# Optimization experiments

Measured on AMD Instinct MI355X. Metric: run time of the kernel, lower is better.

Reference implementation:

```python
import jax, jax.numpy as jnp
import numpy as np

S, B, E, H = 2048, 2, 1024, 16
HD = E // H


def setup_inputs() -> dict:
    key = jax.random.key(0)
    ks = jax.random.split(key, 8)
    sc = 0.05
    return {
        "query": jax.random.normal(ks[0], (S, B, E), jnp.float32),
        "key": jax.random.normal(ks[1], (S, B, E), jnp.float32),
        "value": jax.random.normal(ks[2], (S, B, E), jnp.float32),
        "position_bias": jax.random.normal(ks[3], (B, S, S), jnp.float32) * sc,
        "in_proj_weight": jax.random.normal(ks[4], (3 * E, E), jnp.float32) * sc,
        "in_proj_bias": jnp.zeros((3 * E,), jnp.float32),
        "out_w": jax.random.normal(ks[5], (E, E), jnp.float32) * sc,
        "out_b": jnp.zeros((E,), jnp.float32),
    }


def reference(query, key, value, position_bias, in_proj_weight, in_proj_bias, out_w, out_b):
    # packed in-projection: w is (3E, E) in q,k,v order
    w_q, w_k, w_v = jnp.split(in_proj_weight, 3, axis=0)
    b_q, b_k, b_v = jnp.split(in_proj_bias, 3, axis=0)
    q = query @ w_q.T + b_q          # (S, B, E)
    k = key @ w_k.T + b_k
    v = value @ w_v.T + b_v
    # split heads: (S, B, H, HD)
    q = q.reshape(S, B, H, HD)
    k = k.reshape(S, B, H, HD)
    v = v.reshape(S, B, H, HD)
    scale = 1.0 / jnp.sqrt(jnp.float32(HD))
    # scores: (B, H, tgt, src)
    scores = jnp.einsum("qbhd,kbhd->bhqk", q * scale, k)
    scores = scores + position_bias[:, None, :, :]
    attn = jax.nn.softmax(scores, axis=-1)
    out = jnp.einsum("bhqk,kbhd->qbhd", attn, v).reshape(S, B, E)
    out = out @ out_w.T + out_b      # (S, B, E)
    attn_weights = attn.reshape(B * H, S, S)
    return out, attn_weights
```

## Files before the change

kernel.cpp:

```cpp
#include <hip/hip_runtime.h>

#define S_ 2048
#define B_ 2
#define E_ 1024
#define H_ 16

typedef _Float16 f16x8 __attribute__((ext_vector_type(8)));
typedef _Float16 f16x4 __attribute__((ext_vector_type(4)));
typedef _Float16 f16x2 __attribute__((ext_vector_type(2)));
typedef float f32x4 __attribute__((ext_vector_type(4)));
typedef unsigned short us4_t __attribute__((ext_vector_type(4)));
typedef unsigned u32x4 __attribute__((ext_vector_type(4)));
typedef unsigned u32x2 __attribute__((ext_vector_type(2)));

static __device__ __forceinline__ unsigned short f2h(float x) {
  _Float16 h = (_Float16)x;
  return __builtin_bit_cast(unsigned short, h);
}
static __device__ __forceinline__ unsigned pk_f16(float a, float b) {
  auto r = __builtin_amdgcn_cvt_pkrtz(a, b);
  return __builtin_bit_cast(unsigned, r);
}

__global__ void k_cvth(const float* __restrict__ src, unsigned short* __restrict__ dst, int n4) {
  int i = blockIdx.x * blockDim.x + threadIdx.x;
  int st = gridDim.x * blockDim.x;
  for (; i < n4; i += st) {
    f32x4 x = ((const f32x4*)src)[i];
    us4_t h;
    #pragma unroll
    for (int j = 0; j < 4; ++j) h[j] = f2h(x[j]);
    ((us4_t*)dst)[i] = h;
  }
}

__launch_bounds__(256, 2)
__global__ void k_proj_qk(const unsigned short* __restrict__ qx, const unsigned short* __restrict__ kx,
                          const unsigned short* __restrict__ wqk, const float* __restrict__ bias,
                          unsigned short* __restrict__ qf, unsigned short* __restrict__ kf) {
  const int z = blockIdx.z;
  const unsigned short* A = z ? kx : qx;
  const unsigned short* W = wqk + (size_t)z * (1024 * 1024);
  unsigned short* C = z ? kf : qf;
  const float* bia = bias + z * 1024;
  const float scale = z ? 1.0f : 0.125f;

  __shared__ unsigned short sA[128][40], sB[128][40];

  const int t = threadIdx.x;
  const int wid = t >> 6, l = t & 63, g = l >> 4, c = l & 15;
  const int wr = wid >> 1, wc = wid & 1;
  const int mb = blockIdx.x * 128, nb = blockIdx.y * 128;
  const int sr = t >> 1, sc = (t & 1) * 16;

  f32x4 acc[4][4] = {};

  for (int k0 = 0; k0 < 1024; k0 += 32) {
    __syncthreads();
    {
      const unsigned short* pa = A + (size_t)(mb + sr) * 1024 + k0 + sc;
      const unsigned short* pb = W + (size_t)(nb + sr) * 1024 + k0 + sc;
      *(f16x8*)&sA[sr][sc]     = *(const f16x8*)pa;
      *(f16x8*)&sA[sr][sc + 8] = *(const f16x8*)(pa + 8);
      *(f16x8*)&sB[sr][sc]     = *(const f16x8*)pb;
      *(f16x8*)&sB[sr][sc + 8] = *(const f16x8*)(pb + 8);
    }
    __syncthreads();
    f16x8 af[4], bf[4];
    #pragma unroll
    for (int i = 0; i < 4; ++i) {
      af[i] = *(const f16x8*)&sA[wr * 64 + i * 16 + c][g * 8];
      bf[i] = *(const f16x8*)&sB[wc * 64 + i * 16 + c][g * 8];
    }
    #pragma unroll
    for (int i = 0; i < 4; ++i)
      #pragma unroll
      for (int j = 0; j < 4; ++j)
        acc[i][j] = __builtin_amdgcn_mfma_f32_16x16x32_f16(af[i], bf[j], acc[i][j], 0, 0, 0);
  }
  #pragma unroll
  for (int i = 0; i < 4; ++i)
    #pragma unroll
    for (int j = 0; j < 4; ++j)
      #pragma unroll
      for (int rr = 0; rr < 4; ++rr) {
        int m = mb + wr * 64 + i * 16 + 4 * g + rr;
        int n = nb + wc * 64 + j * 16 + c;
        float v = (acc[i][j][rr] + bia[n]) * scale;
        C[(size_t)m * 1024 + n] = f2h(v);
      }
}

__launch_bounds__(256, 2)
__global__ void k_proj_v(const unsigned short* __restrict__ wv, const unsigned short* __restrict__ vx,
                         const float* __restrict__ bias, unsigned short* __restrict__ VT) {
  __shared__ unsigned short sA[128][40], sB[128][40];
  const int t = threadIdx.x;
  const int wid = t >> 6, l = t & 63, g = l >> 4, c = l & 15;
  const int wr = wid >> 1, wc = wid & 1;
  const int mb = blockIdx.x * 128;
  const int nb = blockIdx.y * 128;
  const int bb = nb >> 11;
  const int jb = nb & 2047;
  const int sr = t >> 1, sc = (t & 1) * 16;

  f32x4 acc[4][4] = {};
  for (int k0 = 0; k0 < 1024; k0 += 32) {
    __syncthreads();
    {
      const unsigned short* pa = wv + (size_t)(mb + sr) * 1024 + k0 + sc;
      const unsigned short* pb = vx + ((size_t)(jb + sr) * 2 + bb) * 1024 + k0 + sc;
      *(f16x8*)&sA[sr][sc]     = *(const f16x8*)pa;
      *(f16x8*)&sA[sr][sc + 8] = *(const f16x8*)(pa + 8);
      *(f16x8*)&sB[sr][sc]     = *(const f16x8*)pb;
      *(f16x8*)&sB[sr][sc + 8] = *(const f16x8*)(pb + 8);
    }
    __syncthreads();
    f16x8 af[4], bf[4];
    #pragma unroll
    for (int i = 0; i < 4; ++i) {
      af[i] = *(const f16x8*)&sA[wr * 64 + i * 16 + c][g * 8];
      bf[i] = *(const f16x8*)&sB[wc * 64 + i * 16 + c][g * 8];
    }
    #pragma unroll
    for (int i = 0; i < 4; ++i)
      #pragma unroll
      for (int j = 0; j < 4; ++j)
        acc[i][j] = __builtin_amdgcn_mfma_f32_16x16x32_f16(af[i], bf[j], acc[i][j], 0, 0, 0);
  }
  #pragma unroll
  for (int i = 0; i < 4; ++i)
    #pragma unroll
    for (int j = 0; j < 4; ++j)
      #pragma unroll
      for (int rr = 0; rr < 4; ++rr) {
        int m = mb + wr * 64 + i * 16 + 4 * g + rr;
        int jj = jb + wc * 64 + j * 16 + c;
        float v = acc[i][j][rr] + bias[2048 + m];
        VT[(size_t)bb * (1024 * 2048) + (size_t)m * 2048 + jj] = f2h(v);
      }
}

__launch_bounds__(256, 3)
__global__ void k_attn_pv(const unsigned short* __restrict__ qf, const unsigned short* __restrict__ kf,
                          const unsigned short* __restrict__ VT, const float* __restrict__ posb,
                          float* __restrict__ attn, unsigned short* __restrict__ oc) {
  const int swz = (int)((blockIdx.x & 7) * 512 + (blockIdx.x >> 3));
  const int h = swz >> 8;
  const int b = (swz >> 7) & 1;
  const int qt = swz & 127;

  const int t = threadIdx.x;
  const int wid = t >> 6, l = t & 63, g = l >> 4, c = l & 15;
  const int ct = wid;

  __shared__ unsigned smem[8192];
  __shared__ float lds_red[4][16];
  unsigned* S_k = smem;
  unsigned* S_v = smem + 4096;

  const size_t qoff = ((size_t)(qt * 16 + c) * 2 + b) * 1024 + h * 64 + g * 8;
  const f16x8 qfr0 = *(const f16x8*)(qf + qoff);
  const f16x8 qfr1 = *(const f16x8*)(qf + qoff + 32);

  const unsigned short* kfb = kf + (size_t)b * 1024 + h * 64;
  const unsigned short* vtb = VT + ((size_t)b * 1024 + h * 64) * 2048;
  const float* pbRow = posb + (size_t)b * S_ * S_ + (size_t)(qt * 16 + c) * S_ + ct * 16;

  const int rb = t >> 3;
  const int lsl = (t & 7) ^ (rb & 7);

  #define LDSRD(base, row, slot) \
    __builtin_bit_cast(f16x8, *(const u32x4*)&(base)[(row) * 32 + ((((slot) ^ ((row) & 7))) * 4)])

  #define GLOAD(dst, stg) do { \
    dst[0] = *(const u32x4*)(kfb + (size_t)((stg) * 64 + rb) * 2048 + lsl * 8); \
    dst[1] = *(const u32x4*)(kfb + (size_t)((stg) * 64 + rb + 32) * 2048 + lsl * 8); \
    dst[2] = *(const u32x4*)(vtb + (size_t)rb * 2048 + (stg) * 64 + lsl * 8); \
    dst[3] = *(const u32x4*)(vtb + (size_t)(rb + 32) * 2048 + (stg) * 64 + lsl * 8); \
  } while (0)

  #define SWRITE(src, buf) do { \
    *(u32x4*)&S_k[(buf) * 2048 + t * 4]        = src[0]; \
    *(u32x4*)&S_k[(buf) * 2048 + 1024 + t * 4] = src[1]; \
    *(u32x4*)&S_v[(buf) * 2048 + t * 4]        = src[2]; \
    *(u32x4*)&S_v[(buf) * 2048 + 1024 + t * 4] = src[3]; \
  } while (0)

  u32x4 rg[3][4];
  f32x4 bias[2];
  unsigned psc0[32], psc1[32];
  float lsum = 0.f;
  f32x4 oacc[4] = {};

  GLOAD(rg[0], 0);
  SWRITE(rg[0], 0);
  GLOAD(rg[1], 1);
  GLOAD(rg[2], 2);
  {
    f32x4 b0 = *(const f32x4*)(pbRow + 4 * g);
    bias[0][0] = b0[0] - 8.f; bias[0][1] = b0[1] - 8.f;
    bias[0][2] = b0[2] - 8.f; bias[0][3] = b0[3] - 8.f;
  }
  __syncthreads();

  #pragma unroll
  for (int st = 0; st < 32; ++st) {
    const int cur = st & 1;
    if (st < 29) GLOAD(rg[st % 3], st + 3);
    if (st < 31) {
      f32x4 bb = *(const f32x4*)(pbRow + (st + 1) * 64 + 4 * g);
      bias[cur ^ 1][0] = bb[0] - 8.f; bias[cur ^ 1][1] = bb[1] - 8.f;
      bias[cur ^ 1][2] = bb[2] - 8.f; bias[cur ^ 1][3] = bb[3] - 8.f;
    }

    {
      const int row = ct * 16 + c;
      const unsigned* kb = S_k + cur * 2048;
      f16x8 kfr0 = LDSRD(kb, row, g);
      f16x8 kfr1 = LDSRD(kb, row, 4 + g);
      f32x4 aA = {}, aB = {};
      aA = __builtin_amdgcn_mfma_f32_16x16x32_f16(kfr0, qfr0, aA, 0, 0, 0);
      aB = __builtin_amdgcn_mfma_f32_16x16x32_f16(kfr1, qfr1, aB, 0, 0, 0);
      float p0 = __expf(aA[0] + aB[0] + bias[cur][0]);
      float p1 = __expf(aA[1] + aB[1] + bias[cur][1]);
      float p2 = __expf(aA[2] + aB[2] + bias[cur][2]);
      float p3 = __expf(aA[3] + aB[3] + bias[cur][3]);
      lsum += (p0 + p1) + (p2 + p3);
      psc0[st] = pk_f16(p0, p1);
      psc1[st] = pk_f16(p2, p3);
    }

    {
      u32x2 br; br[0] = psc0[st]; br[1] = psc1[st];
      const f16x4 bfrag = __builtin_bit_cast(f16x4, br);
      const unsigned* vb = S_v + cur * 2048;
      #pragma unroll
      for (int dt = 0; dt < 4; ++dt) {
        const int row = dt * 16 + c;
        const int sl = (2 * ct + (g >> 1)) ^ (row & 7);
        u32x2 ar = *(const u32x2*)&vb[row * 32 + sl * 4 + 2 * (g & 1)];
        f32x4 o = oacc[dt];
#if __has_builtin(__builtin_amdgcn_mfma_f32_16x16x16f16)
        o = __builtin_amdgcn_mfma_f32_16x16x16f16(__builtin_bit_cast(f16x4, ar), bfrag, o, 0, 0, 0);
#else
        asm("v_mfma_f32_16x16x16_f16 %0, %1, %2, %0" : "+v"(o) : "v"(__builtin_bit_cast(f16x4, ar)), "v"(bfrag));
#endif
        oacc[dt] = o;
      }
    }

    if (st < 31) SWRITE(rg[(st + 1) % 3], cur ^ 1);
    __syncthreads();
  }

  lsum += __shfl_xor(lsum, 16, 64);
  lsum += __shfl_xor(lsum, 32, 64);
  if (l < 16) lds_red[wid][l] = lsum;
  __syncthreads();
  const float inv = 1.0f / ((lds_red[0][c] + lds_red[1][c]) + (lds_red[2][c] + lds_red[3][c]));

  float* ored = (float*)smem;
  #pragma unroll
  for (int dt = 0; dt < 4; ++dt) {
    f32x4 o = oacc[dt];
    o[0] *= inv; o[1] *= inv; o[2] *= inv; o[3] *= inv;
    *(f32x4*)&ored[(wid * 16 + c) * 68 + dt * 16 + 4 * g] = o;
  }
  __syncthreads();
  {
    const int q = t >> 4;
    const int d0 = (t & 15) * 4;
    f32x4 s0 = *(const f32x4*)&ored[(0 * 16 + q) * 68 + d0];
    f32x4 s1 = *(const f32x4*)&ored[(1 * 16 + q) * 68 + d0];
    f32x4 s2 = *(const f32x4*)&ored[(2 * 16 + q) * 68 + d0];
    f32x4 s3 = *(const f32x4*)&ored[(3 * 16 + q) * 68 + d0];
    f32x4 s;
    s[0] = (s0[0] + s1[0]) + (s2[0] + s3[0]);
    s[1] = (s0[1] + s1[1]) + (s2[1] + s3[1]);
    s[2] = (s0[2] + s1[2]) + (s2[2] + s3[2]);
    s[3] = (s0[3] + s1[3]) + (s2[3] + s3[3]);
    u32x2 pk;
    pk[0] = pk_f16(s[0], s[1]);
    pk[1] = pk_f16(s[2], s[3]);
    *(u32x2*)&oc[((size_t)(qt * 16 + q) * 2 + b) * 1024 + h * 64 + d0] = pk;
  }

  float* arow = attn + ((size_t)(b * 16 + h) * S_ + qt * 16 + c) * S_ + ct * 16;
  #pragma unroll
  for (int st = 0; st < 32; ++st) {
    f16x2 h0 = __builtin_bit_cast(f16x2, psc0[st]);
    f16x2 h1 = __builtin_bit_cast(f16x2, psc1[st]);
    f32x4 o;
    o[0] = (float)h0[0] * inv;
    o[1] = (float)h0[1] * inv;
    o[2] = (float)h1[0] * inv;
    o[3] = (float)h1[1] * inv;
    *(f32x4*)(arow + (size_t)st * 64 + 4 * g) = o;
  }
  #undef LDSRD
  #undef GLOAD
  #undef SWRITE
}

__launch_bounds__(256, 2)
__global__ void k_outproj(const unsigned short* __restrict__ oc, const unsigned short* __restrict__ ow,
                          const float* __restrict__ ob, float* __restrict__ out) {
  __shared__ unsigned short sA[128][40], sB[128][40];
  const int t = threadIdx.x;
  const int wid = t >> 6, l = t & 63, g = l >> 4, c = l & 15;
  const int wr = wid >> 1, wc = wid & 1;
  const int mb = blockIdx.x * 128, nb = blockIdx.y * 128;
  const int sr = t >> 1, sc = (t & 1) * 16;

  f32x4 acc[4][4] = {};
  for (int k0 = 0; k0 < 1024; k0 += 32) {
    __syncthreads();
    {
      const unsigned short* pa = oc + (size_t)(mb + sr) * 1024 + k0 + sc;
      const unsigned short* pb = ow + (size_t)(nb + sr) * 1024 + k0 + sc;
      *(f16x8*)&sA[sr][sc]     = *(const f16x8*)pa;
      *(f16x8*)&sA[sr][sc + 8] = *(const f16x8*)(pa + 8);
      *(f16x8*)&sB[sr][sc]     = *(const f16x8*)pb;
      *(f16x8*)&sB[sr][sc + 8] = *(const f16x8*)(pb + 8);
    }
    __syncthreads();
    f16x8 af[4], bf[4];
    #pragma unroll
    for (int i = 0; i < 4; ++i) {
      af[i] = *(const f16x8*)&sA[wr * 64 + i * 16 + c][g * 8];
      bf[i] = *(const f16x8*)&sB[wc * 64 + i * 16 + c][g * 8];
    }
    #pragma unroll
    for (int i = 0; i < 4; ++i)
      #pragma unroll
      for (int j = 0; j < 4; ++j)
        acc[i][j] = __builtin_amdgcn_mfma_f32_16x16x32_f16(af[i], bf[j], acc[i][j], 0, 0, 0);
  }
  #pragma unroll
  for (int i = 0; i < 4; ++i)
    #pragma unroll
    for (int j = 0; j < 4; ++j)
      #pragma unroll
      for (int rr = 0; rr < 4; ++rr) {
        int m = mb + wr * 64 + i * 16 + 4 * g + rr;
        int n = nb + wc * 64 + j * 16 + c;
        out[(size_t)m * 1024 + n] = acc[i][j][rr] + ob[n];
      }
}

extern "C" void kernel_launch(void* const* d_in, const int* in_sizes, int n_in,
                              void* d_out, int out_size, void* d_ws, size_t ws_size,
                              hipStream_t stream) {
  (void)in_sizes; (void)n_in; (void)out_size; (void)ws_size;
  const float* query = (const float*)d_in[0];
  const float* keyi  = (const float*)d_in[1];
  const float* value = (const float*)d_in[2];
  const float* posb  = (const float*)d_in[3];
  const float* ipw   = (const float*)d_in[4];
  const float* ipb   = (const float*)d_in[5];
  const float* outw  = (const float*)d_in[6];
  const float* outb  = (const float*)d_in[7];
  float* out = (float*)d_out;
  float* attn = out + (size_t)S_ * B_ * E_;

  char* ws = (char*)d_ws;
  size_t off = 0;
  auto alloc = [&](size_t bytes) -> void* {
    void* p = ws + off;
    off += (bytes + 255) & ~(size_t)255;
    return p;
  };
  const size_t NTOK = (size_t)S_ * B_;
  unsigned short* qx  = (unsigned short*)alloc(NTOK * 1024 * 2);
  unsigned short* kx  = (unsigned short*)alloc(NTOK * 1024 * 2);
  unsigned short* vx  = (unsigned short*)alloc(NTOK * 1024 * 2);
  unsigned short* wqk = (unsigned short*)alloc((size_t)2048 * 1024 * 2);
  unsigned short* wv  = (unsigned short*)alloc((size_t)1024 * 1024 * 2);
  unsigned short* ow  = (unsigned short*)alloc((size_t)1024 * 1024 * 2);
  unsigned short* qf  = (unsigned short*)alloc(NTOK * 1024 * 2);
  unsigned short* kf  = (unsigned short*)alloc(NTOK * 1024 * 2);
  unsigned short* VT  = (unsigned short*)alloc((size_t)2 * 1024 * 2048 * 2);
  unsigned short* oc  = (unsigned short*)alloc(NTOK * 1024 * 2);

  const int n1_4 = (int)(NTOK * 1024 / 4);
  k_cvth<<<2048, 256, 0, stream>>>(query, qx, n1_4);
  k_cvth<<<2048, 256, 0, stream>>>(keyi, kx, n1_4);
  k_cvth<<<2048, 256, 0, stream>>>(value, vx, n1_4);
  k_cvth<<<1024, 256, 0, stream>>>(ipw, wqk, 2048 * 1024 / 4);
  k_cvth<<<512, 256, 0, stream>>>(ipw + 2048 * 1024, wv, 1024 * 1024 / 4);
  k_cvth<<<512, 256, 0, stream>>>(outw, ow, 1024 * 1024 / 4);

  k_proj_qk<<<dim3(32, 8, 2), 256, 0, stream>>>(qx, kx, wqk, ipb, qf, kf);
  k_proj_v<<<dim3(8, 32), 256, 0, stream>>>(wv, vx, ipb, VT);
  k_attn_pv<<<4096, 256, 0, stream>>>(qf, kf, VT, posb, attn, oc);
  k_outproj<<<dim3(32, 8), 256, 0, stream>>>(oc, ow, outb, out);
}
```

Measured before the change: 378.3 us.

## Fuse fp32-to-fp16 conversion into GEMM loads and defer PV step in attention

```diff
diff --git a/kernel.cpp b/kernel.cpp
--- a/kernel.cpp
+++ b/kernel.cpp
@@ -22,25 +22,24 @@
   return __builtin_bit_cast(unsigned, r);
 }
 
-__global__ void k_cvth(const float* __restrict__ src, unsigned short* __restrict__ dst, int n4) {
-  int i = blockIdx.x * blockDim.x + threadIdx.x;
-  int st = gridDim.x * blockDim.x;
-  for (; i < n4; i += st) {
-    f32x4 x = ((const f32x4*)src)[i];
-    us4_t h;
-    #pragma unroll
-    for (int j = 0; j < 4; ++j) h[j] = f2h(x[j]);
-    ((us4_t*)dst)[i] = h;
-  }
+static __device__ __forceinline__ void cvt16(const float* __restrict__ p, unsigned* dst) {
+  f32x4 a0 = *(const f32x4*)p;
+  f32x4 a1 = *(const f32x4*)(p + 4);
+  f32x4 a2 = *(const f32x4*)(p + 8);
+  f32x4 a3 = *(const f32x4*)(p + 12);
+  dst[0] = pk_f16(a0[0], a0[1]); dst[1] = pk_f16(a0[2], a0[3]);
+  dst[2] = pk_f16(a1[0], a1[1]); dst[3] = pk_f16(a1[2], a1[3]);
+  dst[4] = pk_f16(a2[0], a2[1]); dst[5] = pk_f16(a2[2], a2[3]);
+  dst[6] = pk_f16(a3[0], a3[1]); dst[7] = pk_f16(a3[2], a3[3]);
 }
 
 __launch_bounds__(256, 2)
-__global__ void k_proj_qk(const unsigned short* __restrict__ qx, const unsigned short* __restrict__ kx,
-                          const unsigned short* __restrict__ wqk, const float* __restrict__ bias,
+__global__ void k_proj_qk(const float* __restrict__ query, const float* __restrict__ keyi,
+                          const float* __restrict__ ipw, const float* __restrict__ bias,
                           unsigned short* __restrict__ qf, unsigned short* __restrict__ kf) {
   const int z = blockIdx.z;
-  const unsigned short* A = z ? kx : qx;
-  const unsigned short* W = wqk + (size_t)z * (1024 * 1024);
+  const float* A = z ? keyi : query;
+  const float* W = ipw + (size_t)z * (1024 * 1024);
   unsigned short* C = z ? kf : qf;
   const float* bia = bias + z * 1024;
   const float scale = z ? 1.0f : 0.125f;
@@ -58,12 +57,13 @@
   for (int k0 = 0; k0 < 1024; k0 += 32) {
     __syncthreads();
     {
-      const unsigned short* pa = A + (size_t)(mb + sr) * 1024 + k0 + sc;
-      const unsigned short* pb = W + (size_t)(nb + sr) * 1024 + k0 + sc;
-      *(f16x8*)&sA[sr][sc]     = *(const f16x8*)pa;
-      *(f16x8*)&sA[sr][sc + 8] = *(const f16x8*)(pa + 8);
-      *(f16x8*)&sB[sr][sc]     = *(const f16x8*)pb;
-      *(f16x8*)&sB[sr][sc + 8] = *(const f16x8*)(pb + 8);
+      unsigned ap[8], bp[8];
+      cvt16(A + (size_t)(mb + sr) * 1024 + k0 + sc, ap);
+      cvt16(W + (size_t)(nb + sr) * 1024 + k0 + sc, bp);
+      *(u32x4*)&sA[sr][sc]     = *(u32x4*)&ap[0];
+      *(u32x4*)&sA[sr][sc + 8] = *(u32x4*)&ap[4];
+      *(u32x4*)&sB[sr][sc]     = *(u32x4*)&bp[0];
+      *(u32x4*)&sB[sr][sc + 8] = *(u32x4*)&bp[4];
     }
     __syncthreads();
     f16x8 af[4], bf[4];
@@ -92,7 +92,7 @@
 }
 
 __launch_bounds__(256, 2)
-__global__ void k_proj_v(const unsigned short* __restrict__ wv, const unsigned short* __restrict__ vx,
+__global__ void k_proj_v(const float* __restrict__ ipw, const float* __restrict__ value,
                          const float* __restrict__ bias, unsigned short* __restrict__ VT) {
   __shared__ unsigned short sA[128][40], sB[128][40];
   const int t = threadIdx.x;
@@ -103,17 +103,19 @@
   const int bb = nb >> 11;
   const int jb = nb & 2047;
   const int sr = t >> 1, sc = (t & 1) * 16;
+  const float* wv = ipw + (size_t)2048 * 1024;
 
   f32x4 acc[4][4] = {};
   for (int k0 = 0; k0 < 1024; k0 += 32) {
     __syncthreads();
     {
-      const unsigned short* pa = wv + (size_t)(mb + sr) * 1024 + k0 + sc;
-      const unsigned short* pb = vx + ((size_t)(jb + sr) * 2 + bb) * 1024 + k0 + sc;
-      *(f16x8*)&sA[sr][sc]     = *(const f16x8*)pa;
-      *(f16x8*)&sA[sr][sc + 8] = *(const f16x8*)(pa + 8);
-      *(f16x8*)&sB[sr][sc]     = *(const f16x8*)pb;
-      *(f16x8*)&sB[sr][sc + 8] = *(const f16x8*)(pb + 8);
+      unsigned ap[8], bp[8];
+      cvt16(wv + (size_t)(mb + sr) * 1024 + k0 + sc, ap);
+      cvt16(value + ((size_t)(jb + sr) * 2 + bb) * 1024 + k0 + sc, bp);
+      *(u32x4*)&sA[sr][sc]     = *(u32x4*)&ap[0];
+      *(u32x4*)&sA[sr][sc + 8] = *(u32x4*)&ap[4];
+      *(u32x4*)&sB[sr][sc]     = *(u32x4*)&bp[0];
+      *(u32x4*)&sB[sr][sc + 8] = *(u32x4*)&bp[4];
     }
     __syncthreads();
     f16x8 af[4], bf[4];
@@ -154,7 +156,7 @@
   const int wid = t >> 6, l = t & 63, g = l >> 4, c = l & 15;
   const int ct = wid;
 
-  __shared__ unsigned smem[8192];
+  __shared__ unsigned smem[10240];
   __shared__ float lds_red[4][16];
   unsigned* S_k = smem;
   unsigned* S_v = smem + 4096;
@@ -180,11 +182,11 @@
     dst[3] = *(const u32x4*)(vtb + (size_t)(rb + 32) * 2048 + (stg) * 64 + lsl * 8); \
   } while (0)
 
-  #define SWRITE(src, buf) do { \
-    *(u32x4*)&S_k[(buf) * 2048 + t * 4]        = src[0]; \
-    *(u32x4*)&S_k[(buf) * 2048 + 1024 + t * 4] = src[1]; \
-    *(u32x4*)&S_v[(buf) * 2048 + t * 4]        = src[2]; \
-    *(u32x4*)&S_v[(buf) * 2048 + 1024 + t * 4] = src[3]; \
+  #define SWRITE(src, kbuf, vbuf) do { \
+    *(u32x4*)&S_k[(kbuf) * 2048 + t * 4]        = src[0]; \
+    *(u32x4*)&S_k[(kbuf) * 2048 + 1024 + t * 4] = src[1]; \
+    *(u32x4*)&S_v[(vbuf) * 2048 + t * 4]        = src[2]; \
+    *(u32x4*)&S_v[(vbuf) * 2048 + 1024 + t * 4] = src[3]; \
   } while (0)
 
   u32x4 rg[3][4];
@@ -193,8 +195,21 @@
   float lsum = 0.f;
   f32x4 oacc[4] = {};
 
+  #define PVSTEP(i) do { \
+    u32x2 br_; br_[0] = psc0[i]; br_[1] = psc1[i]; \
+    const f16x4 bfrag_ = __builtin_bit_cast(f16x4, br_); \
+    const unsigned* vb_ = S_v + ((i) % 3) * 2048; \
+    _Pragma("unroll") \
+    for (int dt = 0; dt < 4; ++dt) { \
+      const int row_ = dt * 16 + c; \
+      const int sl_ = (2 * ct + (g >> 1)) ^ (row_ & 7); \
+      u32x2 ar_ = *(const u32x2*)&vb_[row_ * 32 + sl_ * 4 + 2 * (g & 1)]; \
+      oacc[dt] = __builtin_amdgcn_mfma_f32_16x16x16f16(__builtin_bit_cast(f16x4, ar_), bfrag_, oacc[dt], 0, 0, 0); \
+    } \
+  } while (0)
+
   GLOAD(rg[0], 0);
-  SWRITE(rg[0], 0);
+  SWRITE(rg[0], 0, 0);
   GLOAD(rg[1], 1);
   GLOAD(rg[2], 2);
   {
@@ -231,28 +246,12 @@
       psc1[st] = pk_f16(p2, p3);
     }
 
-    {
-      u32x2 br; br[0] = psc0[st]; br[1] = psc1[st];
-      const f16x4 bfrag = __builtin_bit_cast(f16x4, br);
-      const unsigned* vb = S_v + cur * 2048;
-      #pragma unroll
-      for (int dt = 0; dt < 4; ++dt) {
-        const int row = dt * 16 + c;
-        const int sl = (2 * ct + (g >> 1)) ^ (row & 7);
-        u32x2 ar = *(const u32x2*)&vb[row * 32 + sl * 4 + 2 * (g & 1)];
-        f32x4 o = oacc[dt];
-#if __has_builtin(__builtin_amdgcn_mfma_f32_16x16x16f16)
-        o = __builtin_amdgcn_mfma_f32_16x16x16f16(__builtin_bit_cast(f16x4, ar), bfrag, o, 0, 0, 0);
-#else
-        asm("v_mfma_f32_16x16x16_f16 %0, %1, %2, %0" : "+v"(o) : "v"(__builtin_bit_cast(f16x4, ar)), "v"(bfrag));
-#endif
-        oacc[dt] = o;
-      }
-    }
-
-    if (st < 31) SWRITE(rg[(st + 1) % 3], cur ^ 1);
-    __syncthreads();
-  }
+    if (st >= 1) PVSTEP(st - 1);
+
+    if (st < 31) SWRITE(rg[(st + 1) % 3], (st + 1) & 1, (st + 1) % 3);
+    __syncthreads();
+  }
+  PVSTEP(31);
 
   lsum += __shfl_xor(lsum, 16, 64);
   lsum += __shfl_xor(lsum, 32, 64);
@@ -301,10 +300,11 @@
   #undef LDSRD
   #undef GLOAD
   #undef SWRITE
+  #undef PVSTEP
 }
 
 __launch_bounds__(256, 2)
-__global__ void k_outproj(const unsigned short* __restrict__ oc, const unsigned short* __restrict__ ow,
+__global__ void k_outproj(const unsigned short* __restrict__ oc, const float* __restrict__ outw,
                           const float* __restrict__ ob, float* __restrict__ out) {
   __shared__ unsigned short sA[128][40], sB[128][40];
   const int t = threadIdx.x;
@@ -318,11 +318,12 @@
     __syncthreads();
     {
       const unsigned short* pa = oc + (size_t)(mb + sr) * 1024 + k0 + sc;
-      const unsigned short* pb = ow + (size_t)(nb + sr) * 1024 + k0 + sc;
+      unsigned bp[8];
+      cvt16(outw + (size_t)(nb + sr) * 1024 + k0 + sc, bp);
       *(f16x8*)&sA[sr][sc]     = *(const f16x8*)pa;
       *(f16x8*)&sA[sr][sc + 8] = *(const f16x8*)(pa + 8);
-      *(f16x8*)&sB[sr][sc]     = *(const f16x8*)pb;
-      *(f16x8*)&sB[sr][sc + 8] = *(const f16x8*)(pb + 8);
+      *(u32x4*)&sB[sr][sc]     = *(u32x4*)&bp[0];
+      *(u32x4*)&sB[sr][sc + 8] = *(u32x4*)&bp[4];
     }
     __syncthreads();
     f16x8 af[4], bf[4];
@@ -372,27 +373,13 @@
     return p;
   };
   const size_t NTOK = (size_t)S_ * B_;
-  unsigned short* qx  = (unsigned short*)alloc(NTOK * 1024 * 2);
-  unsigned short* kx  = (unsigned short*)alloc(NTOK * 1024 * 2);
-  unsigned short* vx  = (unsigned short*)alloc(NTOK * 1024 * 2);
-  unsigned short* wqk = (unsigned short*)alloc((size_t)2048 * 1024 * 2);
-  unsigned short* wv  = (unsigned short*)alloc((size_t)1024 * 1024 * 2);
-  unsigned short* ow  = (unsigned short*)alloc((size_t)1024 * 1024 * 2);
-  unsigned short* qf  = (unsigned short*)alloc(NTOK * 1024 * 2);
-  unsigned short* kf  = (unsigned short*)alloc(NTOK * 1024 * 2);
-  unsigned short* VT  = (unsigned short*)alloc((size_t)2 * 1024 * 2048 * 2);
-  unsigned short* oc  = (unsigned short*)alloc(NTOK * 1024 * 2);
-
-  const int n1_4 = (int)(NTOK * 1024 / 4);
-  k_cvth<<<2048, 256, 0, stream>>>(query, qx, n1_4);
-  k_cvth<<<2048, 256, 0, stream>>>(keyi, kx, n1_4);
-  k_cvth<<<2048, 256, 0, stream>>>(value, vx, n1_4);
-  k_cvth<<<1024, 256, 0, stream>>>(ipw, wqk, 2048 * 1024 / 4);
-  k_cvth<<<512, 256, 0, stream>>>(ipw + 2048 * 1024, wv, 1024 * 1024 / 4);
-  k_cvth<<<512, 256, 0, stream>>>(outw, ow, 1024 * 1024 / 4);
-
-  k_proj_qk<<<dim3(32, 8, 2), 256, 0, stream>>>(qx, kx, wqk, ipb, qf, kf);
-  k_proj_v<<<dim3(8, 32), 256, 0, stream>>>(wv, vx, ipb, VT);
+  unsigned short* qf = (unsigned short*)alloc(NTOK * 1024 * 2);
+  unsigned short* kf = (unsigned short*)alloc(NTOK * 1024 * 2);
+  unsigned short* VT = (unsigned short*)alloc((size_t)2 * 1024 * 2048 * 2);
+  unsigned short* oc = (unsigned short*)alloc(NTOK * 1024 * 2);
+
+  k_proj_qk<<<dim3(32, 8, 2), 256, 0, stream>>>(query, keyi, ipw, ipb, qf, kf);
+  k_proj_v<<<dim3(8, 32), 256, 0, stream>>>(ipw, value, ipb, VT);
   k_attn_pv<<<4096, 256, 0, stream>>>(qf, kf, VT, posb, attn, oc);
-  k_outproj<<<dim3(32, 8), 256, 0, stream>>>(oc, ow, outb, out);
-}
+  k_outproj<<<dim3(32, 8), 256, 0, stream>>>(oc, outw, outb, out);
+}
```

New measurement: 413.2 us. +9.2%, slower.

## Skew PV MFMA one stage behind QK and triple-buffer V tiles in LDS

Applied to the files above, without the earlier changes.

```diff
diff --git a/kernel.cpp b/kernel.cpp
--- a/kernel.cpp
+++ b/kernel.cpp
@@ -154,7 +154,7 @@
   const int wid = t >> 6, l = t & 63, g = l >> 4, c = l & 15;
   const int ct = wid;
 
-  __shared__ unsigned smem[8192];
+  __shared__ unsigned smem[10240];
   __shared__ float lds_red[4][16];
   unsigned* S_k = smem;
   unsigned* S_v = smem + 4096;
@@ -180,11 +180,11 @@
     dst[3] = *(const u32x4*)(vtb + (size_t)(rb + 32) * 2048 + (stg) * 64 + lsl * 8); \
   } while (0)
 
-  #define SWRITE(src, buf) do { \
-    *(u32x4*)&S_k[(buf) * 2048 + t * 4]        = src[0]; \
-    *(u32x4*)&S_k[(buf) * 2048 + 1024 + t * 4] = src[1]; \
-    *(u32x4*)&S_v[(buf) * 2048 + t * 4]        = src[2]; \
-    *(u32x4*)&S_v[(buf) * 2048 + 1024 + t * 4] = src[3]; \
+  #define SWRITE(src, kbuf, vbuf) do { \
+    *(u32x4*)&S_k[(kbuf) * 2048 + t * 4]        = src[0]; \
+    *(u32x4*)&S_k[(kbuf) * 2048 + 1024 + t * 4] = src[1]; \
+    *(u32x4*)&S_v[(vbuf) * 2048 + t * 4]        = src[2]; \
+    *(u32x4*)&S_v[(vbuf) * 2048 + 1024 + t * 4] = src[3]; \
   } while (0)
 
   u32x4 rg[3][4];
@@ -193,8 +193,21 @@
   float lsum = 0.f;
   f32x4 oacc[4] = {};
 
+  #define PVSTEP(i) do { \
+    u32x2 br_; br_[0] = psc0[i]; br_[1] = psc1[i]; \
+    const f16x4 bfrag_ = __builtin_bit_cast(f16x4, br_); \
+    const unsigned* vb_ = S_v + ((i) % 3) * 2048; \
+    _Pragma("unroll") \
+    for (int dt = 0; dt < 4; ++dt) { \
+      const int row_ = dt * 16 + c; \
+      const int sl_ = (2 * ct + (g >> 1)) ^ (row_ & 7); \
+      u32x2 ar_ = *(const u32x2*)&vb_[row_ * 32 + sl_ * 4 + 2 * (g & 1)]; \
+      oacc[dt] = __builtin_amdgcn_mfma_f32_16x16x16f16(__builtin_bit_cast(f16x4, ar_), bfrag_, oacc[dt], 0, 0, 0); \
+    } \
+  } while (0)
+
   GLOAD(rg[0], 0);
-  SWRITE(rg[0], 0);
+  SWRITE(rg[0], 0, 0);
   GLOAD(rg[1], 1);
   GLOAD(rg[2], 2);
   {
@@ -231,28 +244,12 @@
       psc1[st] = pk_f16(p2, p3);
     }
 
-    {
-      u32x2 br; br[0] = psc0[st]; br[1] = psc1[st];
-      const f16x4 bfrag = __builtin_bit_cast(f16x4, br);
-      const unsigned* vb = S_v + cur * 2048;
-      #pragma unroll
-      for (int dt = 0; dt < 4; ++dt) {
-        const int row = dt * 16 + c;
-        const int sl = (2 * ct + (g >> 1)) ^ (row & 7);
-        u32x2 ar = *(const u32x2*)&vb[row * 32 + sl * 4 + 2 * (g & 1)];
-        f32x4 o = oacc[dt];
-#if __has_builtin(__builtin_amdgcn_mfma_f32_16x16x16f16)
-        o = __builtin_amdgcn_mfma_f32_16x16x16f16(__builtin_bit_cast(f16x4, ar), bfrag, o, 0, 0, 0);
-#else
-        asm("v_mfma_f32_16x16x16_f16 %0, %1, %2, %0" : "+v"(o) : "v"(__builtin_bit_cast(f16x4, ar)), "v"(bfrag));
-#endif
-        oacc[dt] = o;
-      }
-    }
-
-    if (st < 31) SWRITE(rg[(st + 1) % 3], cur ^ 1);
-    __syncthreads();
-  }
+    if (st >= 1) PVSTEP(st - 1);
+
+    if (st < 31) SWRITE(rg[(st + 1) % 3], (st + 1) & 1, (st + 1) % 3);
+    __syncthreads();
+  }
+  PVSTEP(31);
 
   lsum += __shfl_xor(lsum, 16, 64);
   lsum += __shfl_xor(lsum, 32, 64);
@@ -301,6 +298,7 @@
   #undef LDSRD
   #undef GLOAD
   #undef SWRITE
+  #undef PVSTEP
 }
 
 __launch_bounds__(256, 2)
```

New measurement: 386.6 us. +2.2%, slower.

## Use direct global-to-LDS loads in attention and merge conversion kernels

Applied to the files above, without the earlier changes.

```diff
diff --git a/kernel.cpp b/kernel.cpp
--- a/kernel.cpp
+++ b/kernel.cpp
@@ -22,15 +22,29 @@
   return __builtin_bit_cast(unsigned, r);
 }
 
-__global__ void k_cvth(const float* __restrict__ src, unsigned short* __restrict__ dst, int n4) {
+__global__ void k_cvt_all(const float* __restrict__ q, const float* __restrict__ k,
+                          const float* __restrict__ v, const float* __restrict__ ipw,
+                          const float* __restrict__ outw,
+                          unsigned short* __restrict__ qx, unsigned short* __restrict__ kx,
+                          unsigned short* __restrict__ vx, unsigned short* __restrict__ w3,
+                          unsigned short* __restrict__ ow) {
+  const int M1 = 1 << 20;
   int i = blockIdx.x * blockDim.x + threadIdx.x;
-  int st = gridDim.x * blockDim.x;
-  for (; i < n4; i += st) {
-    f32x4 x = ((const f32x4*)src)[i];
+  int stp = gridDim.x * blockDim.x;
+  for (; i < 4 * M1; i += stp) {
+    const float* src;
+    unsigned short* dst;
+    int j;
+    if (i < M1)            { src = q;    dst = qx; j = i; }
+    else if (i < 2 * M1)   { src = k;    dst = kx; j = i - M1; }
+    else if (i < 3 * M1)   { src = v;    dst = vx; j = i - 2 * M1; }
+    else if (i < 3 * M1 + 786432) { src = ipw; dst = w3; j = i - 3 * M1; }
+    else                   { src = outw; dst = ow; j = i - 3 * M1 - 786432; }
+    f32x4 x = ((const f32x4*)src)[j];
     us4_t h;
     #pragma unroll
-    for (int j = 0; j < 4; ++j) h[j] = f2h(x[j]);
-    ((us4_t*)dst)[i] = h;
+    for (int e = 0; e < 4; ++e) h[e] = f2h(x[e]);
+    ((us4_t*)dst)[j] = h;
   }
 }
 
@@ -141,7 +155,7 @@
       }
 }
 
-__launch_bounds__(256, 3)
+__launch_bounds__(256, 4)
 __global__ void k_attn_pv(const unsigned short* __restrict__ qf, const unsigned short* __restrict__ kf,
                           const unsigned short* __restrict__ VT, const float* __restrict__ posb,
                           float* __restrict__ attn, unsigned short* __restrict__ oc) {
@@ -173,30 +187,27 @@
   #define LDSRD(base, row, slot) \
     __builtin_bit_cast(f16x8, *(const u32x4*)&(base)[(row) * 32 + ((((slot) ^ ((row) & 7))) * 4)])
 
-  #define GLOAD(dst, stg) do { \
-    dst[0] = *(const u32x4*)(kfb + (size_t)((stg) * 64 + rb) * 2048 + lsl * 8); \
-    dst[1] = *(const u32x4*)(kfb + (size_t)((stg) * 64 + rb + 32) * 2048 + lsl * 8); \
-    dst[2] = *(const u32x4*)(vtb + (size_t)rb * 2048 + (stg) * 64 + lsl * 8); \
-    dst[3] = *(const u32x4*)(vtb + (size_t)(rb + 32) * 2048 + (stg) * 64 + lsl * 8); \
+  #define GLDS(stg, buf) do { \
+    __builtin_amdgcn_global_load_lds( \
+        (const __attribute__((address_space(1))) unsigned*)(kfb + (size_t)((stg) * 64 + rb) * 2048 + lsl * 8), \
+        (__attribute__((address_space(3))) unsigned*)&S_k[(buf) * 2048 + wid * 256], 16, 0, 0); \
+    __builtin_amdgcn_global_load_lds( \
+        (const __attribute__((address_space(1))) unsigned*)(kfb + (size_t)((stg) * 64 + rb + 32) * 2048 + lsl * 8), \
+        (__attribute__((address_space(3))) unsigned*)&S_k[(buf) * 2048 + 1024 + wid * 256], 16, 0, 0); \
+    __builtin_amdgcn_global_load_lds( \
+        (const __attribute__((address_space(1))) unsigned*)(vtb + (size_t)rb * 2048 + (stg) * 64 + lsl * 8), \
+        (__attribute__((address_space(3))) unsigned*)&S_v[(buf) * 2048 + wid * 256], 16, 0, 0); \
+    __builtin_amdgcn_global_load_lds( \
+        (const __attribute__((address_space(1))) unsigned*)(vtb + (size_t)(rb + 32) * 2048 + (stg) * 64 + lsl * 8), \
+        (__attribute__((address_space(3))) unsigned*)&S_v[(buf) * 2048 + 1024 + wid * 256], 16, 0, 0); \
   } while (0)
 
-  #define SWRITE(src, buf) do { \
-    *(u32x4*)&S_k[(buf) * 2048 + t * 4]        = src[0]; \
-    *(u32x4*)&S_k[(buf) * 2048 + 1024 + t * 4] = src[1]; \
-    *(u32x4*)&S_v[(buf) * 2048 + t * 4]        = src[2]; \
-    *(u32x4*)&S_v[(buf) * 2048 + 1024 + t * 4] = src[3]; \
-  } while (0)
-
-  u32x4 rg[3][4];
   f32x4 bias[2];
   unsigned psc0[32], psc1[32];
   float lsum = 0.f;
   f32x4 oacc[4] = {};
 
-  GLOAD(rg[0], 0);
-  SWRITE(rg[0], 0);
-  GLOAD(rg[1], 1);
-  GLOAD(rg[2], 2);
+  GLDS(0, 0);
   {
     f32x4 b0 = *(const f32x4*)(pbRow + 4 * g);
     bias[0][0] = b0[0] - 8.f; bias[0][1] = b0[1] - 8.f;
@@ -207,7 +218,7 @@
   #pragma unroll
   for (int st = 0; st < 32; ++st) {
     const int cur = st & 1;
-    if (st < 29) GLOAD(rg[st % 3], st + 3);
+    if (st < 31) GLDS(st + 1, cur ^ 1);
     if (st < 31) {
       f32x4 bb = *(const f32x4*)(pbRow + (st + 1) * 64 + 4 * g);
       bias[cur ^ 1][0] = bb[0] - 8.f; bias[cur ^ 1][1] = bb[1] - 8.f;
@@ -240,17 +251,10 @@
         const int row = dt * 16 + c;
         const int sl = (2 * ct + (g >> 1)) ^ (row & 7);
         u32x2 ar = *(const u32x2*)&vb[row * 32 + sl * 4 + 2 * (g & 1)];
-        f32x4 o = oacc[dt];
-#if __has_builtin(__builtin_amdgcn_mfma_f32_16x16x16f16)
-        o = __builtin_amdgcn_mfma_f32_16x16x16f16(__builtin_bit_cast(f16x4, ar), bfrag, o, 0, 0, 0);
-#else
-        asm("v_mfma_f32_16x16x16_f16 %0, %1, %2, %0" : "+v"(o) : "v"(__builtin_bit_cast(f16x4, ar)), "v"(bfrag));
-#endif
-        oacc[dt] = o;
+        oacc[dt] = __builtin_amdgcn_mfma_f32_16x16x16f16(__builtin_bit_cast(f16x4, ar), bfrag, oacc[dt], 0, 0, 0);
       }
     }
 
-    if (st < 31) SWRITE(rg[(st + 1) % 3], cur ^ 1);
     __syncthreads();
   }
 
@@ -299,8 +303,7 @@
     *(f32x4*)(arow + (size_t)st * 64 + 4 * g) = o;
   }
   #undef LDSRD
-  #undef GLOAD
-  #undef SWRITE
+  #undef GLDS
 }
 
 __launch_bounds__(256, 2)
@@ -375,24 +378,17 @@
   unsigned short* qx  = (unsigned short*)alloc(NTOK * 1024 * 2);
   unsigned short* kx  = (unsigned short*)alloc(NTOK * 1024 * 2);
   unsigned short* vx  = (unsigned short*)alloc(NTOK * 1024 * 2);
-  unsigned short* wqk = (unsigned short*)alloc((size_t)2048 * 1024 * 2);
-  unsigned short* wv  = (unsigned short*)alloc((size_t)1024 * 1024 * 2);
+  unsigned short* w3  = (unsigned short*)alloc((size_t)3072 * 1024 * 2);
   unsigned short* ow  = (unsigned short*)alloc((size_t)1024 * 1024 * 2);
   unsigned short* qf  = (unsigned short*)alloc(NTOK * 1024 * 2);
   unsigned short* kf  = (unsigned short*)alloc(NTOK * 1024 * 2);
   unsigned short* VT  = (unsigned short*)alloc((size_t)2 * 1024 * 2048 * 2);
   unsigned short* oc  = (unsigned short*)alloc(NTOK * 1024 * 2);
 
-  const int n1_4 = (int)(NTOK * 1024 / 4);
-  k_cvth<<<2048, 256, 0, stream>>>(query, qx, n1_4);
-  k_cvth<<<2048, 256, 0, stream>>>(keyi, kx, n1_4);
-  k_cvth<<<2048, 256, 0, stream>>>(value, vx, n1_4);
-  k_cvth<<<1024, 256, 0, stream>>>(ipw, wqk, 2048 * 1024 / 4);
-  k_cvth<<<512, 256, 0, stream>>>(ipw + 2048 * 1024, wv, 1024 * 1024 / 4);
-  k_cvth<<<512, 256, 0, stream>>>(outw, ow, 1024 * 1024 / 4);
-
-  k_proj_qk<<<dim3(32, 8, 2), 256, 0, stream>>>(qx, kx, wqk, ipb, qf, kf);
-  k_proj_v<<<dim3(8, 32), 256, 0, stream>>>(wv, vx, ipb, VT);
+  k_cvt_all<<<2048, 256, 0, stream>>>(query, keyi, value, ipw, outw, qx, kx, vx, w3, ow);
+
+  k_proj_qk<<<dim3(32, 8, 2), 256, 0, stream>>>(qx, kx, w3, ipb, qf, kf);
+  k_proj_v<<<dim3(8, 32), 256, 0, stream>>>(w3 + (size_t)2048 * 1024, vx, ipb, VT);
   k_attn_pv<<<4096, 256, 0, stream>>>(qf, kf, VT, posb, attn, oc);
   k_outproj<<<dim3(32, 8), 256, 0, stream>>>(oc, ow, outb, out);
 }
```

Result: faster. 363.3 us (-4.0%).
